# Kernel tuning notes

Hardware: AMD Instinct MI355X
Metric: run time of the kernel (lower is better)

The kernel has to match this reference:

```python
import jax, jax.numpy as jnp
import numpy as np
from jax import lax

EPS = 1e-12  # torch F.normalize eps


def _l2norm(x):
    n = jnp.linalg.norm(x, axis=-1, keepdims=True)
    return x / jnp.maximum(n, EPS)


def _conv1x1(x, w):
    # x: [B,C,H,W], w: [O,C] (1x1 conv, no bias)
    return jnp.einsum('bchw,oc->bohw', x, w)


def _se(x, w1, w2):
    # AdaptiveAvgPool2d(1) -> 1x1 conv (no bias) -> ReLU -> 1x1 conv (no bias) -> ReLU
    p = jnp.mean(x, axis=(2, 3))                      # [B,256]
    h = jax.nn.relu(jnp.einsum('bc,oc->bo', p, w1))   # [B,320]
    return jax.nn.relu(jnp.einsum('bc,oc->bo', h, w2))  # [B,1280]


def _tdec(x, wk_w, wk_b, wv_w, wv_b, red_w, rise_w, rise_b):
    # fc_reduce: 1x1 conv 256->128
    x1 = _conv1x1(x, red_w)                           # [B,128,H,W]
    B, d, H, W = x1.shape
    t = x1.reshape(B, d, H * W).transpose(0, 2, 1)    # [B,N,128] tokens
    # same WK linear produces both q and k (xq == xk in the source)
    k = _l2norm(jnp.einsum('bnd,ed->bne', t, wk_w) + wk_b)  # [B,N,128]
    v = _l2norm(jnp.einsum('bnd,ed->bne', t, wv_w) + wv_b)  # [B,N,128]
    # bmm(wq[B,d,N], wk[B,N,d]) -> [B,d,d] channel gram, temp 30 softmax
    attn = jax.nn.softmax(jnp.einsum('bni,bnj->bij', k, k) * 30.0, axis=-1)
    # bmm(attn[B,d,d], v^T[B,d,N]) -> [B,d,N], reshape back to map
    ot = jnp.einsum('bij,bnj->bin', attn, v).reshape(B, d, H, W)
    return _conv1x1(ot, rise_w) + rise_b[None, :, None, None]


def _fwd(x0, x1, x2, x3, x4, spec_w1, spec_w2, comm_w1, comm_w2,
         pre_w, pre_b, wk1_w, wk1_b, wv1_w, wv1_b, red1_w, rise1_w, rise1_b,
         wk2_w, wk2_b, wv2_w, wv2_b, red2_w, rise2_w, rise2_b):
    xs = jnp.stack([x0, x1, x2, x3, x4])              # [5,B,256,H,W]
    B = x0.shape[0]
    # reduce(lambda x,y: abs(x-y), down_x)
    diff = x0
    for xi in (x1, x2, x3, x4):
        diff = jnp.abs(diff - xi)
    ssum = xs.sum(axis=0)
    wd = jax.nn.softmax(_se(diff, spec_w1, spec_w2).reshape(B, 5, 256), axis=1)
    ws = jax.nn.softmax(_se(ssum, comm_w1, comm_w2).reshape(B, 5, 256), axis=1)
    # v2[i] = x_i*wd_i + x_i*ws_i + x_i ; v3 = sum_i v2[i]
    v3 = jnp.einsum('sbchw,bsc->bchw', xs, wd + ws + 1.0)
    pre = jax.nn.relu(
        lax.conv_general_dilated(v3, pre_w, (1, 1), ((1, 1), (1, 1)),
                                 dimension_numbers=('NCHW', 'OIHW', 'NCHW'))
        + pre_b[None, :, None, None])
    f1 = _tdec(pre, wk1_w, wk1_b, wv1_w, wv1_b, red1_w, rise1_w, rise1_b)
    f3 = _tdec(f1 + v3, wk2_w, wk2_b, wv2_w, wv2_b, red2_w, rise2_w, rise2_b)
    return f1 + f3 + v3


def setup_inputs() -> dict:
    key = jax.random.key(0)
    ks = iter(jax.random.split(key, 40))
    B, C, H, W = 16, 256, 64, 64

    def p(shape, scale=0.05):
        return jax.random.normal(next(ks), shape, jnp.float32) * scale

    inp = {f'x{i}': jax.random.normal(next(ks), (B, C, H, W), jnp.float32) for i in range(5)}
    inp.update(
        spec_w1=p((320, 256)), spec_w2=p((1280, 320)),
        comm_w1=p((320, 256)), comm_w2=p((1280, 320)),
        pre_w=p((256, 256, 3, 3)), pre_b=p((256,)),
        wk1_w=p((128, 128)), wk1_b=p((128,)), wv1_w=p((128, 128)), wv1_b=p((128,)),
        red1_w=p((128, 256)), rise1_w=p((256, 128)), rise1_b=p((256,)),
        wk2_w=p((128, 128)), wk2_b=p((128,)), wv2_w=p((128, 128)), wv2_b=p((128,)),
        red2_w=p((128, 256)), rise2_w=p((256, 128)), rise2_b=p((256,)),
    )
    return inp


def reference(x0, x1, x2, x3, x4, spec_w1, spec_w2, comm_w1, comm_w2,
              pre_w, pre_b, wk1_w, wk1_b, wv1_w, wv1_b, red1_w, rise1_w, rise1_b,
              wk2_w, wk2_b, wv2_w, wv2_b, red2_w, rise2_w, rise2_b):
    return _fwd(x0, x1, x2, x3, x4, spec_w1, spec_w2, comm_w1, comm_w2,
                pre_w, pre_b, wk1_w, wk1_b, wv1_w, wv1_b, red1_w, rise1_w, rise1_b,
                wk2_w, wk2_b, wv2_w, wv2_b, red2_w, rise2_w, rise2_b)
```

## Files before the change

kernel.cpp:

```cpp
#include <hip/hip_runtime.h>

#define DI __device__ __forceinline__

typedef short s16x8 __attribute__((ext_vector_type(8)));
typedef unsigned short u16;
typedef u16 u16x4 __attribute__((ext_vector_type(4)));
typedef u16 u16x8 __attribute__((ext_vector_type(8)));
typedef u16 u16x16 __attribute__((ext_vector_type(16)));
typedef float f32x4 __attribute__((ext_vector_type(4)));
typedef _Float16 f16;
typedef f16 f16x4 __attribute__((ext_vector_type(4)));

DI float bf2f(u16 v) { return __builtin_bit_cast(float, (unsigned)v << 16); }
DI u16 f2bf(float f) {
  unsigned u = __builtin_bit_cast(unsigned, f);
  return (u16)((u + 0x7fffu + ((u >> 16) & 1u)) >> 16);
}

__global__ void k_cast8(u16* __restrict__ dst,
    const float* __restrict__ s0, const float* __restrict__ s1,
    const float* __restrict__ s2, const float* __restrict__ s3,
    const float* __restrict__ s4, const float* __restrict__ s5,
    const float* __restrict__ s6, const float* __restrict__ s7) {
  int i = blockIdx.x * 256 + threadIdx.x;
  const float* src; int base;
  if (i < 32768) { src = s0; base = 0; }
  else if (i < 49152) { src = s1; base = 32768; }
  else if (i < 65536) { src = s2; base = 49152; }
  else if (i < 98304) { src = s3; base = 65536; }
  else if (i < 131072) { src = s4; base = 98304; }
  else if (i < 147456) { src = s5; base = 131072; }
  else if (i < 163840) { src = s6; base = 147456; }
  else { src = s7; base = 163840; }
  dst[i] = f2bf(src[i - base]);
}

__global__ void k_wconv(u16* __restrict__ dst, const float* __restrict__ src) {
  int i = blockIdx.x * 256 + threadIdx.x;
  if (i < 9 * 256 * 256) {
    int tap = i >> 16, rem = i & 65535;
    dst[i] = f2bf(src[(size_t)rem * 9 + tap]);
  }
}

__global__ __launch_bounds__(256) void k_pool(
    const float* __restrict__ x0, const float* __restrict__ x1,
    const float* __restrict__ x2, const float* __restrict__ x3,
    const float* __restrict__ x4, float* __restrict__ pd, float* __restrict__ ps,
    f16* __restrict__ hx1, f16* __restrict__ hx2,
    f16* __restrict__ hx3, f16* __restrict__ hx4) {
  int c = blockIdx.x, b = blockIdx.y;
  size_t ebase = ((size_t)b * 256 + c) * 4096 + threadIdx.x * 4;
  float sd = 0.f, sm = 0.f;
#pragma unroll
  for (int it = 0; it < 4; ++it) {
    size_t off = ebase + it * 1024;
    f32x4 a0 = *(const f32x4*)(x0 + off);
    f32x4 a1 = *(const f32x4*)(x1 + off);
    f32x4 a2 = *(const f32x4*)(x2 + off);
    f32x4 a3 = *(const f32x4*)(x3 + off);
    f32x4 a4 = *(const f32x4*)(x4 + off);
    f16x4 h1, h2, h3, h4;
#pragma unroll
    for (int e = 0; e < 4; ++e) {
      float d = fabsf(a0[e] - a1[e]); d = fabsf(d - a2[e]); d = fabsf(d - a3[e]); d = fabsf(d - a4[e]);
      sd += d; sm += a0[e] + a1[e] + a2[e] + a3[e] + a4[e];
      h1[e] = (f16)a1[e]; h2[e] = (f16)a2[e]; h3[e] = (f16)a3[e]; h4[e] = (f16)a4[e];
    }
    *(f16x4*)(hx1 + off) = h1;
    *(f16x4*)(hx2 + off) = h2;
    *(f16x4*)(hx3 + off) = h3;
    *(f16x4*)(hx4 + off) = h4;
  }
  for (int o = 32; o; o >>= 1) { sd += __shfl_xor(sd, o); sm += __shfl_xor(sm, o); }
  __shared__ float rb[4][2];
  int wv = threadIdx.x >> 6, lane = threadIdx.x & 63;
  if (!lane) { rb[wv][0] = sd; rb[wv][1] = sm; }
  __syncthreads();
  if (!threadIdx.x) {
    float a = rb[0][0] + rb[1][0] + rb[2][0] + rb[3][0];
    float s2 = rb[0][1] + rb[1][1] + rb[2][1] + rb[3][1];
    pd[b * 256 + c] = a * (1.f / 4096.f);
    ps[b * 256 + c] = s2 * (1.f / 4096.f);
  }
}

__global__ __launch_bounds__(256) void k_se1(
    const float* __restrict__ pd, const float* __restrict__ ps,
    const float* __restrict__ sw1, const float* __restrict__ cw1,
    float* __restrict__ h1) {
  int b = blockIdx.y, z = blockIdx.z;
  int wv = threadIdx.x >> 6, lane = threadIdx.x & 63;
  int e = blockIdx.x * 4 + wv;
  const float* in = (z ? ps : pd) + b * 256;
  const float* w = (z ? cw1 : sw1) + (size_t)e * 256;
  float a = 0.f;
#pragma unroll
  for (int i = 0; i < 4; ++i) a += in[lane + 64 * i] * w[lane + 64 * i];
  for (int o = 32; o; o >>= 1) a += __shfl_xor(a, o);
  if (!lane) h1[((size_t)z * 16 + b) * 320 + e] = fmaxf(a, 0.f);
}

__global__ __launch_bounds__(256) void k_se2(
    const float* __restrict__ h1, const float* __restrict__ sw2,
    const float* __restrict__ cw2, float* __restrict__ h2) {
  int b = blockIdx.y, z = blockIdx.z;
  int wv = threadIdx.x >> 6, lane = threadIdx.x & 63;
  int e = blockIdx.x * 4 + wv;
  const float* in = h1 + ((size_t)z * 16 + b) * 320;
  const float* w = (z ? cw2 : sw2) + (size_t)e * 320;
  float a = 0.f;
#pragma unroll
  for (int i = 0; i < 5; ++i) a += in[lane + 64 * i] * w[lane + 64 * i];
  for (int o = 32; o; o >>= 1) a += __shfl_xor(a, o);
  if (!lane) h2[((size_t)z * 16 + b) * 1280 + e] = fmaxf(a, 0.f);
}

__global__ __launch_bounds__(256) void k_se3(
    const float* __restrict__ h2, float* __restrict__ wt) {
  int b = blockIdx.x, t = threadIdx.x;
  const float* Hs = h2 + (size_t)b * 1280;
  const float* Hc = h2 + (size_t)(16 + b) * 1280;
  float d0 = Hs[t], d1 = Hs[256 + t], d2 = Hs[512 + t], d3 = Hs[768 + t], d4 = Hs[1024 + t];
  float m = fmaxf(fmaxf(fmaxf(d0, d1), fmaxf(d2, d3)), d4);
  float e0 = expf(d0 - m), e1 = expf(d1 - m), e2 = expf(d2 - m), e3 = expf(d3 - m), e4 = expf(d4 - m);
  float inv = 1.f / (e0 + e1 + e2 + e3 + e4);
  float c0 = Hc[t], c1 = Hc[256 + t], c2 = Hc[512 + t], c3 = Hc[768 + t], c4 = Hc[1024 + t];
  float mc = fmaxf(fmaxf(fmaxf(c0, c1), fmaxf(c2, c3)), c4);
  float g0 = expf(c0 - mc), g1 = expf(c1 - mc), g2 = expf(c2 - mc), g3 = expf(c3 - mc), g4 = expf(c4 - mc);
  float ci = 1.f / (g0 + g1 + g2 + g3 + g4);
  size_t base = (size_t)b * 1280 + t;
  wt[base + 0 * 256] = e0 * inv + g0 * ci + 1.f;
  wt[base + 1 * 256] = e1 * inv + g1 * ci + 1.f;
  wt[base + 2 * 256] = e2 * inv + g2 * ci + 1.f;
  wt[base + 3 * 256] = e3 * inv + g3 * ci + 1.f;
  wt[base + 4 * 256] = e4 * inv + g4 * ci + 1.f;
}

__global__ __launch_bounds__(256) void k_v3(
    const float* __restrict__ x0, const f16* __restrict__ hx1,
    const f16* __restrict__ hx2, const f16* __restrict__ hx3,
    const f16* __restrict__ hx4, const float* __restrict__ wt,
    u16* __restrict__ v3b) {
  int h = blockIdx.x, b = blockIdx.y;
  __shared__ float W[1280];
  __shared__ u16 T[256][68];
  int t = threadIdx.x;
  for (int s = t; s < 1280; s += 256) W[s] = wt[(size_t)b * 1280 + s];
  __syncthreads();
  int csub = t >> 4, l16 = t & 15;
  size_t ebase = (size_t)b * 256 * 4096 + h * 64 + l16 * 4;
#pragma unroll 4
  for (int ci = 0; ci < 16; ++ci) {
    int c = ci * 16 + csub;
    size_t a = ebase + (size_t)c * 4096;
    f32x4 v0 = *(const f32x4*)(x0 + a);
    f16x4 v1 = *(const f16x4*)(hx1 + a);
    f16x4 v2 = *(const f16x4*)(hx2 + a);
    f16x4 v3 = *(const f16x4*)(hx3 + a);
    f16x4 v4 = *(const f16x4*)(hx4 + a);
    float w0 = W[c], w1 = W[256 + c], w2 = W[512 + c], w3 = W[768 + c], w4 = W[1024 + c];
    u16x4 ov;
#pragma unroll
    for (int e = 0; e < 4; ++e)
      ov[e] = f2bf(v0[e] * w0 + (float)v1[e] * w1 + (float)v2[e] * w2 +
                   (float)v3[e] * w3 + (float)v4[e] * w4);
    *(u16x4*)(&T[c][l16 * 4]) = ov;
  }
  __syncthreads();
  int w = t >> 2, oct = t & 3;
  size_t obase = ((size_t)b * 4096 + h * 64 + w) * 256;
  for (int pass = 0; pass < 8; ++pass) {
    int c0 = oct * 8 + pass * 32;
    u16x8 ov;
#pragma unroll
    for (int jj = 0; jj < 8; ++jj) ov[jj] = T[c0 + jj][w];
    *(u16x8*)(v3b + obase + c0) = ov;
  }
}

__global__ __launch_bounds__(256) void k_conv(
    const u16* __restrict__ v3b, const u16* __restrict__ Wt,
    const float* __restrict__ bias, u16* __restrict__ pre) {
  int o = blockIdx.x;
  int wg = (o & 7) * 128 + (o >> 3);
  int oh = wg & 1, hp = (wg >> 1) & 31, b = wg >> 6;
  __shared__ __align__(16) u16 Ain[4 * 64 * 40];
  __shared__ __align__(16) u16 Bls[2][128 * 40];
  int t = threadIdx.x, wv = t >> 6, lane = t & 63;
  int wm = (wv >> 1) * 64, wn = (wv & 1) * 64, fr = lane & 15, ko = lane >> 4;

  auto loadA = [&](int cc, int s) -> u16x16 {
    int r = s >> 7, rest = s & 127, w = rest >> 1, half = rest & 1;
    int hs = hp * 2 - 1 + r;
    u16x16 v = {};
    if ((unsigned)hs < 64u)
      v = *(const u16x16*)(v3b + (((size_t)b * 64 + hs) * 64 + w) * 256 + cc * 32 + half * 16);
    return v;
  };
  auto storeA = [&](int s, u16x16 v) {
    int r = s >> 7, rest = s & 127, w = rest >> 1, half = rest & 1;
    *(u16x16*)(Ain + (r * 64 + w) * 40 + half * 16) = v;
  };
  auto loadB = [&](int tap, int cc) -> u16x16 {
    int n = t >> 1, half = t & 1;
    return *(const u16x16*)(Wt + ((size_t)tap * 256 + oh * 128 + n) * 256 + cc * 32 + half * 16);
  };
  auto storeB = [&](int bsel, u16x16 v) {
    int n = t >> 1, half = t & 1;
    *(u16x16*)(Bls[bsel] + n * 40 + half * 16) = v;
  };

  u16x16 pA0 = loadA(0, t), pA1 = loadA(0, t + 256);
  u16x16 rB = loadB(0, 0);
  storeA(t, pA0); storeA(t + 256, pA1); storeB(0, rB);
  rB = loadB(1, 0);
  __syncthreads();

  f32x4 acc[4][4] = {};
  int buf = 0;
  for (int cc = 0; cc < 8; ++cc) {
#pragma unroll
    for (int tap = 0; tap < 9; ++tap) {
      const int dh = tap / 3 - 1, dw = tap % 3 - 1;
      s16x8 af[4], bfr[4];
#pragma unroll
      for (int i = 0; i < 4; ++i) {
        int m = wm + i * 16 + fr, r = m >> 6, wq = m & 63;
        int wqd = wq + dw;
        s16x8 v = {};
        if ((unsigned)wqd < 64u)
          v = *(const s16x8*)(Ain + ((r + dh + 1) * 64 + wqd) * 40 + ko * 8);
        af[i] = v;
      }
#pragma unroll
      for (int j = 0; j < 4; ++j)
        bfr[j] = *(const s16x8*)(Bls[buf] + (wn + j * 16 + fr) * 40 + ko * 8);
#pragma unroll
      for (int i = 0; i < 4; ++i)
#pragma unroll
        for (int j = 0; j < 4; ++j)
          acc[i][j] = __builtin_amdgcn_mfma_f32_16x16x32_bf16(af[i], bfr[j], acc[i][j], 0, 0, 0);
      const int u = cc * 9 + tap;
      if (u < 71) {
        if (tap == 8) {
          __syncthreads();
          storeA(t, pA0); storeA(t + 256, pA1);
        }
        storeB(buf ^ 1, rB);
        if (u + 2 <= 71) {
          const int un = u + 2;
          rB = loadB(un % 9, un / 9);
        }
        if (tap == 7 && cc < 7) { pA0 = loadA(cc + 1, t); pA1 = loadA(cc + 1, t + 256); }
        __syncthreads();
        buf ^= 1;
      }
    }
  }
#pragma unroll
  for (int i = 0; i < 4; ++i) {
    int m0 = wm + i * 16 + ko * 4;
#pragma unroll
    for (int j = 0; j < 4; ++j) {
      int och = oh * 128 + wn + j * 16 + fr;
      float bv = bias[och];
#pragma unroll
      for (int r = 0; r < 4; ++r) {
        float v = fmaxf(acc[i][j][r] + bv, 0.f);
        pre[((size_t)b * 4096 + hp * 128 + m0 + r) * 256 + och] = f2bf(v);
      }
    }
  }
}

__global__ __launch_bounds__(256) void k_qkv(
    const u16* __restrict__ in,
    const u16* __restrict__ redW,
    const u16* __restrict__ wkW,
    const u16* __restrict__ wvW,
    const float* __restrict__ kb, const float* __restrict__ vb,
    u16* __restrict__ vout,
    u16* __restrict__ khat) {
  int nt = blockIdx.x, b = blockIdx.y;
  const u16* Ab = in + ((size_t)b * 4096 + nt * 128) * 256;
  __shared__ __align__(16) u16 Ald[128 * 40];
  __shared__ __align__(16) u16 Bld[128 * 40];
  __shared__ __align__(16) u16 T[128 * 136];
  __shared__ float SS[2][128];
  int t = threadIdx.x, wv = t >> 6, lane = t & 63;
  int wm = (wv >> 1) * 64, wn = (wv & 1) * 64, fr = lane & 15, ko = lane >> 4;
  f32x4 acc[4][4] = {};
  for (int kc = 0; kc < 256; kc += 32) {
    for (int s = t; s < 512; s += 256) {
      int r = s >> 2, ks = s & 3;
      *(u16x8*)(Ald + r * 40 + ks * 8) = *(const u16x8*)(Ab + (size_t)r * 256 + kc + ks * 8);
    }
    for (int s = t; s < 512; s += 256) {
      int r = s >> 2, ks = s & 3;
      *(u16x8*)(Bld + r * 40 + ks * 8) = *(const u16x8*)(redW + (size_t)r * 256 + kc + ks * 8);
    }
    __syncthreads();
    s16x8 af[4], bf[4];
#pragma unroll
    for (int i = 0; i < 4; ++i) af[i] = *(const s16x8*)(Ald + (wm + i * 16 + fr) * 40 + ko * 8);
#pragma unroll
    for (int j = 0; j < 4; ++j) bf[j] = *(const s16x8*)(Bld + (wn + j * 16 + fr) * 40 + ko * 8);
#pragma unroll
    for (int i = 0; i < 4; ++i)
#pragma unroll
      for (int j = 0; j < 4; ++j)
        acc[i][j] = __builtin_amdgcn_mfma_f32_16x16x32_bf16(af[i], bf[j], acc[i][j], 0, 0, 0);
    __syncthreads();
  }
#pragma unroll
  for (int i = 0; i < 4; ++i)
#pragma unroll
    for (int j = 0; j < 4; ++j)
#pragma unroll
      for (int r = 0; r < 4; ++r)
        T[(wm + i * 16 + ko * 4 + r) * 136 + wn + j * 16 + fr] = f2bf(acc[i][j][r]);

  for (int z = 0; z < 2; ++z) {
    const u16* W = z ? wkW : wvW;
    const float* bias = z ? kb : vb;
    f32x4 a2[4][4] = {};
#pragma unroll
    for (int h = 0; h < 2; ++h) {
      __syncthreads();
      for (int s = t; s < 512; s += 256) {
        int r = s >> 2, ks = s & 3;
        *(u16x8*)(Ald + r * 40 + ks * 8) = *(const u16x8*)(W + (size_t)r * 128 + h * 64 + ks * 8);
      }
      for (int s = t; s < 512; s += 256) {
        int r = s >> 2, ks = s & 3;
        *(u16x8*)(Bld + r * 40 + ks * 8) = *(const u16x8*)(W + (size_t)r * 128 + h * 64 + 32 + ks * 8);
      }
      __syncthreads();
#pragma unroll
      for (int kk = 0; kk < 2; ++kk) {
        const u16* Bsrc = kk ? Bld : Ald;
        s16x8 af[4], bf[4];
#pragma unroll
        for (int i = 0; i < 4; ++i)
          af[i] = *(const s16x8*)(T + (size_t)(wm + i * 16 + fr) * 136 + h * 64 + kk * 32 + ko * 8);
#pragma unroll
        for (int j = 0; j < 4; ++j)
          bf[j] = *(const s16x8*)(Bsrc + (wn + j * 16 + fr) * 40 + ko * 8);
#pragma unroll
        for (int i = 0; i < 4; ++i)
#pragma unroll
          for (int j = 0; j < 4; ++j)
            a2[i][j] = __builtin_amdgcn_mfma_f32_16x16x32_bf16(af[i], bf[j], a2[i][j], 0, 0, 0);
      }
    }
    float bj[4];
#pragma unroll
    for (int j = 0; j < 4; ++j) bj[j] = bias[wn + j * 16 + fr];
    float pss[4][4];
#pragma unroll
    for (int i = 0; i < 4; ++i)
#pragma unroll
      for (int r = 0; r < 4; ++r) pss[i][r] = 0.f;
#pragma unroll
    for (int i = 0; i < 4; ++i)
#pragma unroll
      for (int j = 0; j < 4; ++j)
#pragma unroll
        for (int r = 0; r < 4; ++r) {
          float v = a2[i][j][r] + bj[j];
          a2[i][j][r] = v;
          pss[i][r] += v * v;
        }
#pragma unroll
    for (int m = 1; m < 16; m <<= 1)
#pragma unroll
      for (int i = 0; i < 4; ++i)
#pragma unroll
        for (int r = 0; r < 4; ++r) pss[i][r] += __shfl_xor(pss[i][r], m);
    if (fr == 0)
#pragma unroll
      for (int i = 0; i < 4; ++i)
#pragma unroll
        for (int r = 0; r < 4; ++r) SS[wv & 1][wm + i * 16 + ko * 4 + r] = pss[i][r];
    __syncthreads();
    float sc[4][4];
#pragma unroll
    for (int i = 0; i < 4; ++i)
#pragma unroll
      for (int r = 0; r < 4; ++r) {
        int tok = wm + i * 16 + ko * 4 + r;
        float s2 = SS[0][tok] + SS[1][tok];
        sc[i][r] = 1.f / fmaxf(sqrtf(s2), 1e-12f);
      }
#pragma unroll
    for (int i = 0; i < 4; ++i)
#pragma unroll
      for (int j = 0; j < 4; ++j)
#pragma unroll
        for (int r = 0; r < 4; ++r) a2[i][j][r] *= sc[i][r];
    if (z == 0) {
      size_t tokbase = (size_t)b * 4096 + nt * 128;
#pragma unroll
      for (int i = 0; i < 4; ++i)
#pragma unroll
        for (int j = 0; j < 4; ++j) {
          u16* dst = vout + (tokbase + wm + i * 16 + ko * 4) * 128 + wn + j * 16 + fr;
#pragma unroll
          for (int r = 0; r < 4; ++r) dst[(size_t)r * 128] = f2bf(a2[i][j][r]);
        }
    } else {
#pragma unroll
      for (int i = 0; i < 4; ++i)
#pragma unroll
        for (int j = 0; j < 4; ++j)
#pragma unroll
          for (int r = 0; r < 4; ++r)
            T[(size_t)(wn + j * 16 + fr) * 136 + wm + i * 16 + ko * 4 + r] = f2bf(a2[i][j][r]);
      __syncthreads();
      for (int s = t; s < 2048; s += 256) {
        int ch = s >> 4, sg = s & 15;
        *(u16x8*)(khat + ((size_t)b * 128 + ch) * 4096 + nt * 128 + sg * 8) =
            *(const u16x8*)(T + ch * 136 + sg * 8);
      }
    }
  }
}

template <int MODE>
__global__ __launch_bounds__(256) void k_gemm(
    const u16* __restrict__ A, int lda, const u16* __restrict__ B0,
    const u16* __restrict__ B1, int ldb, int K,
    const float* __restrict__ bias0, const float* __restrict__ bias1,
    u16* __restrict__ out0, u16* __restrict__ out1,
    const u16* __restrict__ add0, const u16* __restrict__ add1,
    float* __restrict__ outf) {
  int nt = blockIdx.x, b = blockIdx.y, z = blockIdx.z;
  const u16* Ab = A + ((size_t)b * 4096 + nt * 128) * (size_t)lda;
  const u16* Bb;
  if constexpr (MODE == 2) Bb = B0 + (size_t)b * 128 * ldb;
  else Bb = B0 + (size_t)z * 128 * ldb;
  __shared__ __align__(16) u16 Ald[128 * 40];
  __shared__ __align__(16) u16 Bld[128 * 40];
  int t = threadIdx.x, wv = t >> 6, lane = t & 63;
  int wm = (wv >> 1) * 64, wn = (wv & 1) * 64, fr = lane & 15, ko = lane >> 4;
  f32x4 acc[4][4] = {};
  for (int kc = 0; kc < K; kc += 32) {
    for (int s = t; s < 512; s += 256) {
      int r = s >> 2, ks = s & 3;
      *(u16x8*)(Ald + r * 40 + ks * 8) = *(const u16x8*)(Ab + (size_t)r * lda + kc + ks * 8);
    }
    for (int s = t; s < 512; s += 256) {
      int r = s >> 2, ks = s & 3;
      *(u16x8*)(Bld + r * 40 + ks * 8) = *(const u16x8*)(Bb + (size_t)r * ldb + kc + ks * 8);
    }
    __syncthreads();
    s16x8 af[4], bf[4];
#pragma unroll
    for (int i = 0; i < 4; ++i) af[i] = *(const s16x8*)(Ald + (wm + i * 16 + fr) * 40 + ko * 8);
#pragma unroll
    for (int j = 0; j < 4; ++j) bf[j] = *(const s16x8*)(Bld + (wn + j * 16 + fr) * 40 + ko * 8);
#pragma unroll
    for (int i = 0; i < 4; ++i)
#pragma unroll
      for (int j = 0; j < 4; ++j)
        acc[i][j] = __builtin_amdgcn_mfma_f32_16x16x32_bf16(af[i], bf[j], acc[i][j], 0, 0, 0);
    __syncthreads();
  }
  size_t tokbase = (size_t)b * 4096 + nt * 128;
#pragma unroll
  for (int i = 0; i < 4; ++i) {
    int m0 = wm + i * 16 + ko * 4;
#pragma unroll
    for (int j = 0; j < 4; ++j) {
      int nc = wn + j * 16 + fr;
      if constexpr (MODE == 2) {
        u16* dst = out0 + (tokbase + m0) * 128 + nc;
#pragma unroll
        for (int r = 0; r < 4; ++r) dst[(size_t)r * 128] = f2bf(acc[i][j][r]);
      } else if constexpr (MODE == 3) {
        int o = z * 128 + nc;
        float bv = bias0[o];
        size_t idx = (tokbase + m0) * 256 + o;
#pragma unroll
        for (int r = 0; r < 4; ++r) {
          float f1v = acc[i][j][r] + bv;
          out0[idx + (size_t)r * 256] = f2bf(f1v);
          out1[idx + (size_t)r * 256] = f2bf(f1v + bf2f(add0[idx + (size_t)r * 256]));
        }
      } else {
        int o = z * 128 + nc;
        float bv = bias0[o];
        size_t idx = (tokbase + m0) * 256 + o;
        f32x4 vv;
#pragma unroll
        for (int r = 0; r < 4; ++r)
          vv[r] = acc[i][j][r] + bv + bf2f(add0[idx + (size_t)r * 256]) + bf2f(add1[idx + (size_t)r * 256]);
        *(f32x4*)(outf + ((size_t)b * 256 + o) * 4096 + nt * 128 + m0) = vv;
      }
    }
  }
}

__global__ __launch_bounds__(256) void k_gram(const u16* __restrict__ kt, float* __restrict__ gp) {
  int ks = blockIdx.x, b = blockIdx.y;
  const u16* base = kt + (size_t)b * 128 * 4096 + ks * 256;
  __shared__ __align__(16) u16 Tld[128 * 40];
  int t = threadIdx.x, wv = t >> 6, lane = t & 63;
  int wm = (wv >> 1) * 64, wn = (wv & 1) * 64, fr = lane & 15, ko = lane >> 4;
  f32x4 acc[4][4] = {};
  for (int kc = 0; kc < 256; kc += 32) {
    for (int s = t; s < 512; s += 256) {
      int r = s >> 2, k2 = s & 3;
      *(u16x8*)(Tld + r * 40 + k2 * 8) = *(const u16x8*)(base + (size_t)r * 4096 + kc + k2 * 8);
    }
    __syncthreads();
    s16x8 af[4], bf[4];
#pragma unroll
    for (int i = 0; i < 4; ++i) af[i] = *(const s16x8*)(Tld + (wm + i * 16 + fr) * 40 + ko * 8);
#pragma unroll
    for (int j = 0; j < 4; ++j) bf[j] = *(const s16x8*)(Tld + (wn + j * 16 + fr) * 40 + ko * 8);
#pragma unroll
    for (int i = 0; i < 4; ++i)
#pragma unroll
      for (int j = 0; j < 4; ++j)
        acc[i][j] = __builtin_amdgcn_mfma_f32_16x16x32_bf16(af[i], bf[j], acc[i][j], 0, 0, 0);
    __syncthreads();
  }
  float* dst = gp + ((size_t)(ks * 16 + b) * 128) * 128;
#pragma unroll
  for (int i = 0; i < 4; ++i) {
    int m0 = wm + i * 16 + ko * 4;
#pragma unroll
    for (int j = 0; j < 4; ++j) {
      int nc = wn + j * 16 + fr;
#pragma unroll
      for (int r = 0; r < 4; ++r) dst[(size_t)(m0 + r) * 128 + nc] = acc[i][j][r];
    }
  }
}

__global__ void k_soft(const float* __restrict__ gp, u16* __restrict__ attn) {
  int i = blockIdx.x, b = blockIdx.y, l = threadIdx.x;
  float s0 = 0.f, s1 = 0.f;
  for (int ks = 0; ks < 16; ++ks) {
    const float* row = gp + (((size_t)ks * 16 + b) * 128 + i) * 128;
    s0 += row[l]; s1 += row[l + 64];
  }
  s0 *= 30.f; s1 *= 30.f;
  float m = fmaxf(s0, s1);
  for (int o = 32; o; o >>= 1) m = fmaxf(m, __shfl_xor(m, o));
  float e0 = expf(s0 - m), e1 = expf(s1 - m);
  float s = e0 + e1;
  for (int o = 32; o; o >>= 1) s += __shfl_xor(s, o);
  float inv = 1.f / s;
  u16* dst = attn + ((size_t)b * 128 + i) * 128;
  dst[l] = f2bf(e0 * inv);
  dst[l + 64] = f2bf(e1 * inv);
}

extern "C" void kernel_launch(void* const* d_in, const int* in_sizes, int n_in,
                              void* d_out, int out_size, void* d_ws, size_t ws_size,
                              hipStream_t stream) {
  (void)in_sizes; (void)n_in; (void)out_size; (void)ws_size;
  const float* x0 = (const float*)d_in[0];
  const float* x1 = (const float*)d_in[1];
  const float* x2 = (const float*)d_in[2];
  const float* x3 = (const float*)d_in[3];
  const float* x4 = (const float*)d_in[4];
  const float* spec_w1 = (const float*)d_in[5];
  const float* spec_w2 = (const float*)d_in[6];
  const float* comm_w1 = (const float*)d_in[7];
  const float* comm_w2 = (const float*)d_in[8];
  const float* pre_w = (const float*)d_in[9];
  const float* pre_bias = (const float*)d_in[10];
  const float* wk1_w = (const float*)d_in[11];
  const float* wk1_b = (const float*)d_in[12];
  const float* wv1_w = (const float*)d_in[13];
  const float* wv1_b = (const float*)d_in[14];
  const float* red1_w = (const float*)d_in[15];
  const float* rise1_w = (const float*)d_in[16];
  const float* rise1_b = (const float*)d_in[17];
  const float* wk2_w = (const float*)d_in[18];
  const float* wk2_b = (const float*)d_in[19];
  const float* wv2_w = (const float*)d_in[20];
  const float* wv2_b = (const float*)d_in[21];
  const float* red2_w = (const float*)d_in[22];
  const float* rise2_w = (const float*)d_in[23];
  const float* rise2_b = (const float*)d_in[24];
  float* out = (float*)d_out;

  char* wsp = (char*)d_ws;
  size_t off = 0;
  auto alloc = [&](size_t bytes) -> void* {
    off = (off + 255) & ~(size_t)255;
    void* p = wsp + off;
    off += bytes;
    return p;
  };
  float* pd = (float*)alloc(16 * 256 * 4);
  float* ps = (float*)alloc(16 * 256 * 4);
  float* h1b = (float*)alloc(2 * 16 * 320 * 4);
  float* h2b = (float*)alloc(2 * 16 * 1280 * 4);
  float* wtb = (float*)alloc(16 * 5 * 256 * 4);
  u16* v3b = (u16*)alloc((size_t)16 * 4096 * 256 * 2);
  u16* Wtc = (u16*)alloc((size_t)9 * 256 * 256 * 2);
  u16* wall = (u16*)alloc((size_t)196608 * 2);
  u16* red1b = wall;
  u16* wk1b = wall + 32768;
  u16* wv1b = wall + 49152;
  u16* rise1b = wall + 65536;
  u16* red2b = wall + 98304;
  u16* wk2b = wall + 131072;
  u16* wv2b = wall + 147456;
  u16* rise2b = wall + 163840;
  u16* pre = (u16*)alloc((size_t)16 * 4096 * 256 * 2);
  u16* tbuf = (u16*)alloc((size_t)16 * 4096 * 128 * 2);
  u16* khat = (u16*)alloc((size_t)16 * 4096 * 128 * 2);
  u16* vbuf = (u16*)alloc((size_t)16 * 4096 * 128 * 2);
  u16* attn = (u16*)alloc((size_t)16 * 128 * 128 * 2);
  u16* Obuf = (u16*)alloc((size_t)16 * 4096 * 128 * 2);
  u16* f1b = (u16*)alloc((size_t)16 * 4096 * 256 * 2);
  float* gpart = (float*)tbuf;
  u16* in2b = pre;
  f16* hx = (f16*)pre;
  const size_t HXN = (size_t)16 * 256 * 4096;
  f16* hx1 = hx;
  f16* hx2 = hx + HXN;
  f16* hx3 = hx + 2 * HXN;
  f16* hx4 = hx + 3 * HXN;

  k_cast8<<<dim3(768), 256, 0, stream>>>(wall, red1_w, wk1_w, wv1_w, rise1_w,
                                         red2_w, wk2_w, wv2_w, rise2_w);
  k_wconv<<<dim3(2304), 256, 0, stream>>>(Wtc, pre_w);

  k_pool<<<dim3(256, 16), 256, 0, stream>>>(x0, x1, x2, x3, x4, pd, ps, hx1, hx2, hx3, hx4);
  k_se1<<<dim3(80, 16, 2), 256, 0, stream>>>(pd, ps, spec_w1, comm_w1, h1b);
  k_se2<<<dim3(320, 16, 2), 256, 0, stream>>>(h1b, spec_w2, comm_w2, h2b);
  k_se3<<<dim3(16), 256, 0, stream>>>(h2b, wtb);
  k_v3<<<dim3(64, 16), 256, 0, stream>>>(x0, hx1, hx2, hx3, hx4, wtb, v3b);
  k_conv<<<dim3(1024), 256, 0, stream>>>(v3b, Wtc, pre_bias, pre);

  k_qkv<<<dim3(32, 16), 256, 0, stream>>>(pre, red1b, wk1b, wv1b, wk1_b, wv1_b, vbuf, khat);
  k_gram<<<dim3(16, 16), 256, 0, stream>>>(khat, gpart);
  k_soft<<<dim3(128, 16), 64, 0, stream>>>(gpart, attn);
  k_gemm<2><<<dim3(32, 16, 1), 256, 0, stream>>>(vbuf, 128, attn, nullptr, 128, 128,
      nullptr, nullptr, Obuf, nullptr, nullptr, nullptr, nullptr);
  k_gemm<3><<<dim3(32, 16, 2), 256, 0, stream>>>(Obuf, 128, rise1b, nullptr, 128, 128,
      rise1_b, nullptr, f1b, in2b, v3b, nullptr, nullptr);

  k_qkv<<<dim3(32, 16), 256, 0, stream>>>(in2b, red2b, wk2b, wv2b, wk2_b, wv2_b, vbuf, khat);
  k_gram<<<dim3(16, 16), 256, 0, stream>>>(khat, gpart);
  k_soft<<<dim3(128, 16), 64, 0, stream>>>(gpart, attn);
  k_gemm<2><<<dim3(32, 16, 1), 256, 0, stream>>>(vbuf, 128, attn, nullptr, 128, 128,
      nullptr, nullptr, Obuf, nullptr, nullptr, nullptr, nullptr);
  k_gemm<4><<<dim3(32, 16, 2), 256, 0, stream>>>(Obuf, 128, rise2b, nullptr, 128, 128,
      rise2_b, nullptr, nullptr, nullptr, f1b, v3b, out);
}
```

Measured before the change: 469.1 us.

## Fuse attention-times-V GEMM with rise projection into one kernel

Replaces the separate attn·V GEMM and the rise 1x1 projection GEMM with a single kernel. The intermediate O tile (128 tokens x 128 channels) is kept in shared memory as bf16, then multiplied by both halves of the rise weight inside the same block. This removes the Obuf round trip through global memory and two kernel launches per decoder. In exchange it uses more LDS per block, which may lower occupancy, and each block now computes both output halves serially, halving the grid size.

```diff
diff --git a/kernel.cpp b/kernel.cpp
--- a/kernel.cpp
+++ b/kernel.cpp
@@ -428,31 +428,30 @@
 }
 
 template <int MODE>
-__global__ __launch_bounds__(256) void k_gemm(
-    const u16* __restrict__ A, int lda, const u16* __restrict__ B0,
-    const u16* __restrict__ B1, int ldb, int K,
-    const float* __restrict__ bias0, const float* __restrict__ bias1,
-    u16* __restrict__ out0, u16* __restrict__ out1,
+__global__ __launch_bounds__(256) void k_pvrise(
+    const u16* __restrict__ vbuf,
+    const u16* __restrict__ attnb,
+    const u16* __restrict__ riseW,
+    const float* __restrict__ bias,
     const u16* __restrict__ add0, const u16* __restrict__ add1,
-    float* __restrict__ outf) {
-  int nt = blockIdx.x, b = blockIdx.y, z = blockIdx.z;
-  const u16* Ab = A + ((size_t)b * 4096 + nt * 128) * (size_t)lda;
-  const u16* Bb;
-  if constexpr (MODE == 2) Bb = B0 + (size_t)b * 128 * ldb;
-  else Bb = B0 + (size_t)z * 128 * ldb;
+    u16* __restrict__ out0, u16* __restrict__ out1, float* __restrict__ outf) {
+  int nt = blockIdx.x, b = blockIdx.y;
+  const u16* Ab = vbuf + ((size_t)b * 4096 + nt * 128) * 128;
+  const u16* Bb = attnb + (size_t)b * 128 * 128;
   __shared__ __align__(16) u16 Ald[128 * 40];
   __shared__ __align__(16) u16 Bld[128 * 40];
+  __shared__ __align__(16) u16 T[128 * 136];
   int t = threadIdx.x, wv = t >> 6, lane = t & 63;
   int wm = (wv >> 1) * 64, wn = (wv & 1) * 64, fr = lane & 15, ko = lane >> 4;
   f32x4 acc[4][4] = {};
-  for (int kc = 0; kc < K; kc += 32) {
+  for (int kc = 0; kc < 128; kc += 32) {
     for (int s = t; s < 512; s += 256) {
       int r = s >> 2, ks = s & 3;
-      *(u16x8*)(Ald + r * 40 + ks * 8) = *(const u16x8*)(Ab + (size_t)r * lda + kc + ks * 8);
+      *(u16x8*)(Ald + r * 40 + ks * 8) = *(const u16x8*)(Ab + (size_t)r * 128 + kc + ks * 8);
     }
     for (int s = t; s < 512; s += 256) {
       int r = s >> 2, ks = s & 3;
-      *(u16x8*)(Bld + r * 40 + ks * 8) = *(const u16x8*)(Bb + (size_t)r * ldb + kc + ks * 8);
+      *(u16x8*)(Bld + r * 40 + ks * 8) = *(const u16x8*)(Bb + (size_t)r * 128 + kc + ks * 8);
     }
     __syncthreads();
     s16x8 af[4], bf[4];
@@ -467,36 +466,70 @@
         acc[i][j] = __builtin_amdgcn_mfma_f32_16x16x32_bf16(af[i], bf[j], acc[i][j], 0, 0, 0);
     __syncthreads();
   }
+#pragma unroll
+  for (int i = 0; i < 4; ++i)
+#pragma unroll
+    for (int j = 0; j < 4; ++j)
+#pragma unroll
+      for (int r = 0; r < 4; ++r)
+        T[(wm + i * 16 + ko * 4 + r) * 136 + wn + j * 16 + fr] = f2bf(acc[i][j][r]);
+
   size_t tokbase = (size_t)b * 4096 + nt * 128;
-#pragma unroll
-  for (int i = 0; i < 4; ++i) {
-    int m0 = wm + i * 16 + ko * 4;
-#pragma unroll
-    for (int j = 0; j < 4; ++j) {
-      int nc = wn + j * 16 + fr;
-      if constexpr (MODE == 2) {
-        u16* dst = out0 + (tokbase + m0) * 128 + nc;
-#pragma unroll
-        for (int r = 0; r < 4; ++r) dst[(size_t)r * 128] = f2bf(acc[i][j][r]);
-      } else if constexpr (MODE == 3) {
-        int o = z * 128 + nc;
-        float bv = bias0[o];
+  for (int z = 0; z < 2; ++z) {
+    const u16* W = riseW + (size_t)z * 128 * 128;
+    f32x4 a2[4][4] = {};
+#pragma unroll
+    for (int h = 0; h < 2; ++h) {
+      __syncthreads();
+      for (int s = t; s < 512; s += 256) {
+        int r = s >> 2, ks = s & 3;
+        *(u16x8*)(Ald + r * 40 + ks * 8) = *(const u16x8*)(W + (size_t)r * 128 + h * 64 + ks * 8);
+      }
+      for (int s = t; s < 512; s += 256) {
+        int r = s >> 2, ks = s & 3;
+        *(u16x8*)(Bld + r * 40 + ks * 8) = *(const u16x8*)(W + (size_t)r * 128 + h * 64 + 32 + ks * 8);
+      }
+      __syncthreads();
+#pragma unroll
+      for (int kk = 0; kk < 2; ++kk) {
+        const u16* Bsrc = kk ? Bld : Ald;
+        s16x8 af[4], bf[4];
+#pragma unroll
+        for (int i = 0; i < 4; ++i)
+          af[i] = *(const s16x8*)(T + (size_t)(wm + i * 16 + fr) * 136 + h * 64 + kk * 32 + ko * 8);
+#pragma unroll
+        for (int j = 0; j < 4; ++j)
+          bf[j] = *(const s16x8*)(Bsrc + (wn + j * 16 + fr) * 40 + ko * 8);
+#pragma unroll
+        for (int i = 0; i < 4; ++i)
+#pragma unroll
+          for (int j = 0; j < 4; ++j)
+            a2[i][j] = __builtin_amdgcn_mfma_f32_16x16x32_bf16(af[i], bf[j], a2[i][j], 0, 0, 0);
+      }
+    }
+#pragma unroll
+    for (int i = 0; i < 4; ++i) {
+      int m0 = wm + i * 16 + ko * 4;
+#pragma unroll
+      for (int j = 0; j < 4; ++j) {
+        int o = z * 128 + wn + j * 16 + fr;
+        float bv = bias[o];
         size_t idx = (tokbase + m0) * 256 + o;
-#pragma unroll
-        for (int r = 0; r < 4; ++r) {
-          float f1v = acc[i][j][r] + bv;
-          out0[idx + (size_t)r * 256] = f2bf(f1v);
-          out1[idx + (size_t)r * 256] = f2bf(f1v + bf2f(add0[idx + (size_t)r * 256]));
+        if constexpr (MODE == 3) {
+#pragma unroll
+          for (int r = 0; r < 4; ++r) {
+            float f1v = a2[i][j][r] + bv;
+            out0[idx + (size_t)r * 256] = f2bf(f1v);
+            out1[idx + (size_t)r * 256] = f2bf(f1v + bf2f(add0[idx + (size_t)r * 256]));
+          }
+        } else {
+          f32x4 vv;
+#pragma unroll
+          for (int r = 0; r < 4; ++r)
+            vv[r] = a2[i][j][r] + bv + bf2f(add0[idx + (size_t)r * 256]) +
+                    bf2f(add1[idx + (size_t)r * 256]);
+          *(f32x4*)(outf + ((size_t)b * 256 + o) * 4096 + nt * 128 + m0) = vv;
         }
-      } else {
-        int o = z * 128 + nc;
-        float bv = bias0[o];
-        size_t idx = (tokbase + m0) * 256 + o;
-        f32x4 vv;
-#pragma unroll
-        for (int r = 0; r < 4; ++r)
-          vv[r] = acc[i][j][r] + bv + bf2f(add0[idx + (size_t)r * 256]) + bf2f(add1[idx + (size_t)r * 256]);
-        *(f32x4*)(outf + ((size_t)b * 256 + o) * 4096 + nt * 128 + m0) = vv;
       }
     }
   }
@@ -619,8 +652,9 @@
   u16* khat = (u16*)alloc((size_t)16 * 4096 * 128 * 2);
   u16* vbuf = (u16*)alloc((size_t)16 * 4096 * 128 * 2);
   u16* attn = (u16*)alloc((size_t)16 * 128 * 128 * 2);
-  u16* Obuf = (u16*)alloc((size_t)16 * 4096 * 128 * 2);
+  u16* spacer = (u16*)alloc((size_t)16 * 4096 * 128 * 2);
   u16* f1b = (u16*)alloc((size_t)16 * 4096 * 256 * 2);
+  (void)spacer;
   float* gpart = (float*)tbuf;
   u16* in2b = pre;
   f16* hx = (f16*)pre;
@@ -644,16 +678,12 @@
   k_qkv<<<dim3(32, 16), 256, 0, stream>>>(pre, red1b, wk1b, wv1b, wk1_b, wv1_b, vbuf, khat);
   k_gram<<<dim3(16, 16), 256, 0, stream>>>(khat, gpart);
   k_soft<<<dim3(128, 16), 64, 0, stream>>>(gpart, attn);
-  k_gemm<2><<<dim3(32, 16, 1), 256, 0, stream>>>(vbuf, 128, attn, nullptr, 128, 128,
-      nullptr, nullptr, Obuf, nullptr, nullptr, nullptr, nullptr);
-  k_gemm<3><<<dim3(32, 16, 2), 256, 0, stream>>>(Obuf, 128, rise1b, nullptr, 128, 128,
-      rise1_b, nullptr, f1b, in2b, v3b, nullptr, nullptr);
+  k_pvrise<3><<<dim3(32, 16), 256, 0, stream>>>(vbuf, attn, rise1b, rise1_b,
+      v3b, nullptr, f1b, in2b, nullptr);
 
   k_qkv<<<dim3(32, 16), 256, 0, stream>>>(in2b, red2b, wk2b, wv2b, wk2_b, wv2_b, vbuf, khat);
   k_gram<<<dim3(16, 16), 256, 0, stream>>>(khat, gpart);
   k_soft<<<dim3(128, 16), 64, 0, stream>>>(gpart, attn);
-  k_gemm<2><<<dim3(32, 16, 1), 256, 0, stream>>>(vbuf, 128, attn, nullptr, 128, 128,
-      nullptr, nullptr, Obuf, nullptr, nullptr, nullptr, nullptr);
-  k_gemm<4><<<dim3(32, 16, 2), 256, 0, stream>>>(Obuf, 128, rise2b, nullptr, 128, 128,
-      rise2_b, nullptr, nullptr, nullptr, f1b, v3b, out);
-}
+  k_pvrise<4><<<dim3(32, 16), 256, 0, stream>>>(vbuf, attn, rise2b, rise2_b,
+      f1b, v3b, nullptr, nullptr, out);
+}
```

After: 451.5 us. 1.04x faster.
